# Kernel optimization log

Measured on AMD Instinct MI355X. Metric: run time of the kernel, lower is better.

The kernel has to match this reference:

```python
import jax, jax.numpy as jnp
import numpy as np

B, H, W, K, PAD = 1024, 28, 28, 3, 1


def conv3x3(x, w, b):
    out = jax.lax.conv_general_dilated(x, w, (1, 1), ((PAD, PAD), (PAD, PAD)),
                                       dimension_numbers=('NCHW', 'OIHW', 'NCHW'))
    return out + b[None, :, None, None]


def deform_conv2d(x, offset, w, b):
    # torchvision deform_conv2d semantics, stride=1, pad=1, dilation=1, groups=1
    Bn, Cin, Hh, Ww = x.shape
    Cout = w.shape[0]
    KK = K * K
    off = offset.reshape(Bn, KK, 2, Hh, Ww)
    dy, dx = off[:, :, 0], off[:, :, 1]                      # [B,KK,H,W]
    ky, kx = jnp.meshgrid(jnp.arange(K, dtype=x.dtype), jnp.arange(K, dtype=x.dtype), indexing='ij')
    py = dy + (jnp.arange(Hh, dtype=x.dtype) - PAD)[None, None, :, None] + ky.reshape(KK)[None, :, None, None]
    px = dx + (jnp.arange(Ww, dtype=x.dtype) - PAD)[None, None, None, :] + kx.reshape(KK)[None, :, None, None]
    y0 = jnp.floor(py); x0 = jnp.floor(px)
    wy1 = py - y0; wy0 = 1.0 - wy1
    wx1 = px - x0; wx0 = 1.0 - wx1
    xf = x.reshape(Bn, Cin, Hh * Ww)

    def gather(yi, xi):
        valid = (yi >= 0) & (yi < Hh) & (xi >= 0) & (xi < Ww)
        yc = jnp.clip(yi, 0, Hh - 1).astype(jnp.int32)
        xc = jnp.clip(xi, 0, Ww - 1).astype(jnp.int32)
        idx = (yc * Ww + xc).reshape(Bn, -1)                 # [B, KK*H*W]
        g = jnp.take_along_axis(xf, jnp.broadcast_to(idx[:, None, :], (Bn, Cin, idx.shape[1])), axis=2)
        return g.reshape(Bn, Cin, KK, Hh, Ww) * valid.astype(x.dtype)[:, None]

    sampled = (gather(y0, x0) * (wy0 * wx0)[:, None]
               + gather(y0, x0 + 1) * (wy0 * wx1)[:, None]
               + gather(y0 + 1, x0) * (wy1 * wx0)[:, None]
               + gather(y0 + 1, x0 + 1) * (wy1 * wx1)[:, None])  # [B,Cin,KK,H,W]
    out = jnp.einsum('bkhw,ok->bohw', sampled.reshape(Bn, Cin * KK, Hh, Ww),
                     w.reshape(Cout, Cin * KK))
    return out + b[None, :, None, None]


def adaptive_avg_pool_14(x):
    Bn, C, Hh, Ww = x.shape
    f = Hh // 14
    return x.reshape(Bn, C, 14, f, 14, f).mean(axis=(3, 5))


def setup_inputs() -> dict:
    key = jax.random.key(0)
    ks = jax.random.split(key, 14)
    d = {}
    d['x'] = jax.random.normal(ks[0], (B, 1, H, W), dtype=jnp.float32)
    # offset conv 1: Conv2d(1, 18, 3, pad=1)
    d['ow1'] = jax.random.normal(ks[1], (18, 1, 3, 3), dtype=jnp.float32) * 0.1
    d['ob1'] = jnp.zeros((18,), jnp.float32)
    d['w1'] = jax.random.normal(ks[2], (32, 1, 3, 3), dtype=jnp.float32) * 0.01
    d['b1'] = jnp.zeros((32,), jnp.float32)
    # offset conv 2: Conv2d(32, 18, 3, pad=1)
    d['ow2'] = jax.random.normal(ks[3], (18, 32, 3, 3), dtype=jnp.float32) * 0.05
    d['ob2'] = jnp.zeros((18,), jnp.float32)
    d['w2'] = jax.random.normal(ks[4], (64, 32, 3, 3), dtype=jnp.float32) * 0.01
    d['b2'] = jnp.zeros((64,), jnp.float32)
    d['fw1'] = jax.random.normal(ks[5], (128, 64 * 14 * 14), dtype=jnp.float32) * 0.01
    d['fb1'] = jnp.zeros((128,), jnp.float32)
    d['fw2'] = jax.random.normal(ks[6], (10, 128), dtype=jnp.float32) * 0.05
    d['fb2'] = jnp.zeros((10,), jnp.float32)
    return d


def reference(x, ow1, ob1, w1, b1, ow2, ob2, w2, b2, fw1, fb1, fw2, fb2):
    # block1 + relu + pool 28->14
    h = deform_conv2d(x, conv3x3(x, ow1, ob1), w1, b1)
    h = adaptive_avg_pool_14(jax.nn.relu(h))
    # block2 + relu + pool 14->14 (identity)
    h = deform_conv2d(h, conv3x3(h, ow2, ob2), w2, b2)
    h = adaptive_avg_pool_14(jax.nn.relu(h))
    h = h.reshape(h.shape[0], -1)
    # classifier (ExcitationDropout is identity in eval mode)
    h = jax.nn.relu(h @ fw1.T + fb1)
    return h @ fw2.T + fb2
```

## Files before the change

kernel.cpp:

```cpp
#include <hip/hip_runtime.h>

#define NB 1024
#define TOTAL1 (NB*196)
#define SP 208

#define WS_H1   0
#define WS_H2   6422528
#define WS_PART 19267584
#define WS_W1T  23461888
#define WS_OW1T 23462176
#define WS_W2T  23462338
#define WS_OW2T 23480770

__global__ __launch_bounds__(256) void prep(const float* __restrict__ w1,
                                            const float* __restrict__ ow1,
                                            const float* __restrict__ w2,
                                            const float* __restrict__ ow2,
                                            float* __restrict__ ws) {
  int i = blockIdx.x * 256 + threadIdx.x;
  if (i < 288)   { int co = i / 9,  kk = i % 9;   ws[WS_W1T  + kk * 32 + co] = w1[i]; }
  if (i < 162)   { int c  = i / 9,  j  = i % 9;   ws[WS_OW1T + j  * 18 + c ] = ow1[i]; }
  if (i < 18432) { int co = i / 288, k = i % 288; ws[WS_W2T  + k  * 64 + co] = w2[i]; }
  if (i < 5184)  { int c  = i / 288, k = i % 288; ws[WS_OW2T + k  * 18 + c ] = ow2[i]; }
}

__global__ __launch_bounds__(256, 2) void stage1(const float* __restrict__ x,
                                                 const float* __restrict__ ob1,
                                                 const float* __restrict__ b1,
                                                 const float* __restrict__ ws,
                                                 float* __restrict__ h1) {
  __shared__ float ximg[3 * 784];
  const float* __restrict__ w1t  = ws + WS_W1T;
  const float* __restrict__ ow1t = ws + WS_OW1T;
  int tid = threadIdx.x;
  int g0 = blockIdx.x * 256;
  int bfirst = g0 / 196;
  for (int idx = tid; idx < 3 * 784; idx += 256) {
    int img = idx / 784;
    int b = bfirst + img;
    ximg[idx] = (b < NB) ? x[b * 784 + (idx - img * 784)] : 0.f;
  }
  __syncthreads();
  int g = g0 + tid;
  if (g >= TOTAL1) return;
  int b = g / 196, p = g - b * 196;
  const float* im = ximg + (b - bfirst) * 784;
  int oy = p / 14, ox = p - (p / 14) * 14;

  float pooled[32];
#pragma unroll
  for (int co = 0; co < 32; ++co) pooled[co] = 0.f;

  for (int sub = 0; sub < 4; ++sub) {
    int y  = 2 * oy + (sub >> 1);
    int ix = 2 * ox + (sub & 1);
    float patch[9];
#pragma unroll
    for (int j = 0; j < 9; ++j) {
      int yy = y + j / 3 - 1, xc = ix + j % 3 - 1;
      bool ok = (yy >= 0) & (yy < 28) & (xc >= 0) & (xc < 28);
      patch[j] = ok ? im[yy * 28 + xc] : 0.f;
    }
    float off[18];
#pragma unroll
    for (int c = 0; c < 18; ++c) off[c] = ob1[c];
#pragma unroll
    for (int j = 0; j < 9; ++j) {
      float v = patch[j];
#pragma unroll
      for (int c = 0; c < 18; ++c) off[c] = fmaf(v, ow1t[j * 18 + c], off[c]);
    }
    float a[32];
#pragma unroll
    for (int co = 0; co < 32; ++co) a[co] = b1[co];
#pragma unroll
    for (int kk = 0; kk < 9; ++kk) {
      float py = (float)(y - 1 + kk / 3) + off[2 * kk];
      float px = (float)(ix - 1 + kk % 3) + off[2 * kk + 1];
      float y0f = floorf(py), x0f = floorf(px);
      float wy1 = py - y0f, wx1 = px - x0f;
      float wy0 = 1.f - wy1, wx0 = 1.f - wx1;
      int y0 = (int)y0f, x0 = (int)x0f;
      int y1 = y0 + 1, x1 = x0 + 1;
      bool vy0 = (y0 >= 0) & (y0 < 28), vy1 = (y1 >= 0) & (y1 < 28);
      bool vx0 = (x0 >= 0) & (x0 < 28), vx1 = (x1 >= 0) & (x1 < 28);
      float W00 = (vy0 & vx0) ? wy0 * wx0 : 0.f;
      float W01 = (vy0 & vx1) ? wy0 * wx1 : 0.f;
      float W10 = (vy1 & vx0) ? wy1 * wx0 : 0.f;
      float W11 = (vy1 & vx1) ? wy1 * wx1 : 0.f;
      int yc0 = min(max(y0, 0), 27), yc1 = min(max(y1, 0), 27);
      int xc0 = min(max(x0, 0), 27), xc1 = min(max(x1, 0), 27);
      float s = im[yc0 * 28 + xc0] * W00 + im[yc0 * 28 + xc1] * W01 +
                im[yc1 * 28 + xc0] * W10 + im[yc1 * 28 + xc1] * W11;
#pragma unroll
      for (int co = 0; co < 32; ++co) a[co] = fmaf(s, w1t[kk * 32 + co], a[co]);
    }
#pragma unroll
    for (int co = 0; co < 32; ++co) pooled[co] += fmaxf(a[co], 0.f);
  }
#pragma unroll
  for (int co = 0; co < 32; ++co) h1[b * 6272 + co * 196 + p] = pooled[co] * 0.25f;
}

__global__ __launch_bounds__(256, 2) void stage2(const float* __restrict__ h1,
                                                 const float* __restrict__ ob2,
                                                 const float* __restrict__ b2,
                                                 const float* __restrict__ ws,
                                                 float* __restrict__ h2) {
  __shared__ float imgT[196 * 32];
  __shared__ float offs[18 * SP];
  __shared__ float Sbuf[32 * SP];
  const float* __restrict__ w2t  = ws + WS_W2T;
  const float* __restrict__ ow2t = ws + WS_OW2T;
  int tid = threadIdx.x;
  int b = blockIdx.x;

  for (int e = tid; e < 6272; e += 256) {
    int ci = e / 196, p = e - ci * 196;
    imgT[p * 32 + ((ci + 4 * p) & 31)] = h1[b * 6272 + e];
  }

  int pp = tid;
  int spy = pp / 14, spx = pp - (pp / 14) * 14;

  int oc  = tid % 18;
  int opg = tid / 18;
  int op0 = opg * 16;
  bool oact = (tid < 234);
  float oacc[16];
#pragma unroll
  for (int i = 0; i < 16; ++i) oacc[i] = 0.f;

  for (int j = 0; j < 9; ++j) {
    __syncthreads();
    if (pp < SP) {
      if (pp < 196) {
        int yy = spy + j / 3 - 1, xx = spx + j % 3 - 1;
        bool ok = (yy >= 0) & (yy < 14) & (xx >= 0) & (xx < 14);
        int idx = ok ? (yy * 14 + xx) : 0;
        const float* src = imgT + idx * 32;
        int rot = (4 * idx) & 31;
#pragma unroll
        for (int cg = 0; cg < 8; ++cg) {
          float4 v;
          if (ok) v = *(const float4*)(src + ((cg * 4 + rot) & 31));
          else    v = make_float4(0.f, 0.f, 0.f, 0.f);
          Sbuf[(cg * 4 + 0) * SP + pp] = v.x;
          Sbuf[(cg * 4 + 1) * SP + pp] = v.y;
          Sbuf[(cg * 4 + 2) * SP + pp] = v.z;
          Sbuf[(cg * 4 + 3) * SP + pp] = v.w;
        }
      } else {
#pragma unroll
        for (int ci2 = 0; ci2 < 32; ++ci2) Sbuf[ci2 * SP + pp] = 0.f;
      }
    }
    __syncthreads();
    if (oact) {
      float wv[32];
#pragma unroll
      for (int ci2 = 0; ci2 < 32; ++ci2) wv[ci2] = ow2t[(ci2 * 9 + j) * 18 + oc];
      for (int ci2 = 0; ci2 < 32; ++ci2) {
        const float* srow = Sbuf + ci2 * SP + op0;
        float w = wv[ci2];
#pragma unroll
        for (int t = 0; t < 4; ++t) {
          float4 s = *(const float4*)(srow + 4 * t);
          oacc[4 * t + 0] = fmaf(w, s.x, oacc[4 * t + 0]);
          oacc[4 * t + 1] = fmaf(w, s.y, oacc[4 * t + 1]);
          oacc[4 * t + 2] = fmaf(w, s.z, oacc[4 * t + 2]);
          oacc[4 * t + 3] = fmaf(w, s.w, oacc[4 * t + 3]);
        }
      }
    }
  }
  __syncthreads();
  if (oact) {
    float bo = ob2[oc];
#pragma unroll
    for (int i = 0; i < 16; ++i) offs[oc * SP + op0 + i] = oacc[i] + bo;
  }

  int co = tid & 63, pg = tid >> 6;
  int p0 = pg * 52;
  float bb = b2[co];
  float acc[52];
#pragma unroll
  for (int i = 0; i < 52; ++i) acc[i] = bb;

  for (int kk = 0; kk < 9; ++kk) {
    __syncthreads();
    if (pp < SP) {
      if (pp < 196) {
        float dyv = offs[(2 * kk) * SP + pp];
        float dxv = offs[(2 * kk + 1) * SP + pp];
        float pyv = (float)(spy - 1 + kk / 3) + dyv;
        float pxv = (float)(spx - 1 + kk % 3) + dxv;
        float y0f = floorf(pyv), x0f = floorf(pxv);
        float wy1 = pyv - y0f, wx1 = pxv - x0f;
        float wy0 = 1.f - wy1, wx0 = 1.f - wx1;
        int y0 = (int)y0f, x0 = (int)x0f;
        int y1 = y0 + 1, x1 = x0 + 1;
        bool vy0 = (y0 >= 0) & (y0 < 14), vy1 = (y1 >= 0) & (y1 < 14);
        bool vx0 = (x0 >= 0) & (x0 < 14), vx1 = (x1 >= 0) & (x1 < 14);
        float W00 = (vy0 & vx0) ? wy0 * wx0 : 0.f;
        float W01 = (vy0 & vx1) ? wy0 * wx1 : 0.f;
        float W10 = (vy1 & vx0) ? wy1 * wx0 : 0.f;
        float W11 = (vy1 & vx1) ? wy1 * wx1 : 0.f;
        int yc0 = min(max(y0, 0), 13), yc1 = min(max(y1, 0), 13);
        int xc0 = min(max(x0, 0), 13), xc1 = min(max(x1, 0), 13);
        int i00 = yc0 * 14 + xc0, i01 = yc0 * 14 + xc1;
        int i10 = yc1 * 14 + xc0, i11 = yc1 * 14 + xc1;
        const float* s00 = imgT + i00 * 32; int r00 = (4 * i00) & 31;
        const float* s01 = imgT + i01 * 32; int r01 = (4 * i01) & 31;
        const float* s10 = imgT + i10 * 32; int r10 = (4 * i10) & 31;
        const float* s11 = imgT + i11 * 32; int r11 = (4 * i11) & 31;
#pragma unroll
        for (int cg = 0; cg < 8; ++cg) {
          float4 a0 = *(const float4*)(s00 + ((cg * 4 + r00) & 31));
          float4 a1 = *(const float4*)(s01 + ((cg * 4 + r01) & 31));
          float4 a2 = *(const float4*)(s10 + ((cg * 4 + r10) & 31));
          float4 a3 = *(const float4*)(s11 + ((cg * 4 + r11) & 31));
          float vx0v = fmaf(W00, a0.x, fmaf(W01, a1.x, fmaf(W10, a2.x, W11 * a3.x)));
          float vy0v = fmaf(W00, a0.y, fmaf(W01, a1.y, fmaf(W10, a2.y, W11 * a3.y)));
          float vz0v = fmaf(W00, a0.z, fmaf(W01, a1.z, fmaf(W10, a2.z, W11 * a3.z)));
          float vw0v = fmaf(W00, a0.w, fmaf(W01, a1.w, fmaf(W10, a2.w, W11 * a3.w)));
          Sbuf[(cg * 4 + 0) * SP + pp] = vx0v;
          Sbuf[(cg * 4 + 1) * SP + pp] = vy0v;
          Sbuf[(cg * 4 + 2) * SP + pp] = vz0v;
          Sbuf[(cg * 4 + 3) * SP + pp] = vw0v;
        }
      } else {
#pragma unroll
        for (int ci2 = 0; ci2 < 32; ++ci2) Sbuf[ci2 * SP + pp] = 0.f;
      }
    }
    __syncthreads();
    float wv[32];
#pragma unroll
    for (int ci2 = 0; ci2 < 32; ++ci2) wv[ci2] = w2t[(ci2 * 9 + kk) * 64 + co];
#pragma unroll 2
    for (int ci2 = 0; ci2 < 32; ++ci2) {
      const float* srow = Sbuf + ci2 * SP + p0;
      float w = wv[ci2];
#pragma unroll
      for (int t = 0; t < 13; ++t) {
        float4 s = *(const float4*)(srow + 4 * t);
        acc[4 * t + 0] = fmaf(w, s.x, acc[4 * t + 0]);
        acc[4 * t + 1] = fmaf(w, s.y, acc[4 * t + 1]);
        acc[4 * t + 2] = fmaf(w, s.z, acc[4 * t + 2]);
        acc[4 * t + 3] = fmaf(w, s.w, acc[4 * t + 3]);
      }
    }
  }

  for (int half = 0; half < 2; ++half) {
    __syncthreads();
    if ((co >> 5) == half) {
      int cc = co & 31;
#pragma unroll
      for (int i = 0; i < 52; ++i) Sbuf[cc * SP + p0 + i] = acc[i];
    }
    __syncthreads();
    for (int e = tid; e < 6272; e += 256) {
      int cc = e / 196, p = e - cc * 196;
      h2[b * 12544 + (half * 32 + cc) * 196 + p] = fmaxf(Sbuf[cc * SP + p], 0.f);
    }
  }
}

__global__ __launch_bounds__(256, 2) void fc1(const float* __restrict__ h2,
                                              const float* __restrict__ fw1,
                                              float* __restrict__ part) {
  __shared__ float a_s[56 * 72];
  __shared__ float b_s[56 * 132];
  int tid = threadIdx.x;
  int rb = (blockIdx.x & 15) * 64;
  int ks = blockIdx.x >> 4;
  int kbase = ks * 392;
  int c0 = (tid & 31) * 4;
  int r0 = (tid >> 5) * 8;

  float acc[8][4];
#pragma unroll
  for (int i = 0; i < 8; ++i)
#pragma unroll
    for (int j = 0; j < 4; ++j) acc[i][j] = 0.f;

  for (int ch = 0; ch < 7; ++ch) {
    int kb = kbase + ch * 56;
    __syncthreads();
#pragma unroll
    for (int t = 0; t < 14; ++t) {
      int idx = t * 256 + tid;
      int r = idx / 56, k = idx - r * 56;
      a_s[k * 72 + r] = h2[(rb + r) * 12544 + kb + k];
    }
#pragma unroll
    for (int t = 0; t < 28; ++t) {
      int idx = t * 256 + tid;
      int c = idx / 56, k = idx - c * 56;
      b_s[k * 132 + c] = fw1[c * 12544 + kb + k];
    }
    __syncthreads();
    for (int k = 0; k < 56; ++k) {
      float4 bv = *(const float4*)&b_s[k * 132 + c0];
      float4 av0 = *(const float4*)&a_s[k * 72 + r0];
      float4 av1 = *(const float4*)&a_s[k * 72 + r0 + 4];
      float av[8] = {av0.x, av0.y, av0.z, av0.w, av1.x, av1.y, av1.z, av1.w};
      float bj[4] = {bv.x, bv.y, bv.z, bv.w};
#pragma unroll
      for (int i = 0; i < 8; ++i)
#pragma unroll
        for (int j = 0; j < 4; ++j) acc[i][j] = fmaf(av[i], bj[j], acc[i][j]);
    }
  }
#pragma unroll
  for (int i = 0; i < 8; ++i) {
    int r = rb + r0 + i;
#pragma unroll
    for (int j = 0; j < 4; ++j)
      part[(ks * 1024 + r) * 128 + c0 + j] = acc[i][j];
  }
}

__global__ __launch_bounds__(128) void fcfinal(const float* __restrict__ part,
                                               const float* __restrict__ fb1,
                                               const float* __restrict__ fw2,
                                               const float* __restrict__ fb2,
                                               float* __restrict__ out) {
  __shared__ float tbuf[128];
  int b = blockIdx.x, c = threadIdx.x;
  float s = fb1[c];
  for (int ks = 0; ks < 32; ++ks) s += part[(ks * 1024 + b) * 128 + c];
  tbuf[c] = fmaxf(s, 0.f);
  __syncthreads();
  if (c < 10) {
    float v = fb2[c];
#pragma unroll
    for (int k = 0; k < 128; ++k) v = fmaf(tbuf[k], fw2[c * 128 + k], v);
    out[b * 10 + c] = v;
  }
}

extern "C" void kernel_launch(void* const* d_in, const int* in_sizes, int n_in,
                              void* d_out, int out_size, void* d_ws, size_t ws_size,
                              hipStream_t stream) {
  const float* x   = (const float*)d_in[0];
  const float* ow1 = (const float*)d_in[1];
  const float* ob1 = (const float*)d_in[2];
  const float* w1  = (const float*)d_in[3];
  const float* b1  = (const float*)d_in[4];
  const float* ow2 = (const float*)d_in[5];
  const float* ob2 = (const float*)d_in[6];
  const float* w2  = (const float*)d_in[7];
  const float* b2  = (const float*)d_in[8];
  const float* fw1 = (const float*)d_in[9];
  const float* fb1 = (const float*)d_in[10];
  const float* fw2 = (const float*)d_in[11];
  const float* fb2 = (const float*)d_in[12];
  float* ws  = (float*)d_ws;
  float* out = (float*)d_out;

  prep<<<72, 256, 0, stream>>>(w1, ow1, w2, ow2, ws);
  stage1<<<784, 256, 0, stream>>>(x, ob1, b1, ws, ws + WS_H1);
  stage2<<<NB, 256, 0, stream>>>(ws + WS_H1, ob2, b2, ws, ws + WS_H2);
  fc1<<<512, 256, 0, stream>>>(ws + WS_H2, fw1, ws + WS_PART);
  fcfinal<<<1024, 128, 0, stream>>>(ws + WS_PART, fb1, fw2, fb2, out);
}
```

Before: 424.5 us.

## Retile block2 deform-conv GEMM to 4x16 register tiles and store output directly

The block-2 channel-mix GEMM inside the deform conv kernel now gives each thread 4 output channels by 16 pixels instead of 1 channel by 52 pixels. Each shared-memory sample is reused across 4 weights, and the weights are loaded as float4 vectors. The aim is to cut LDS traffic per FMA. The final ReLU store now writes straight from registers to global memory with float4 stores, which removes the two-pass shared-memory staging and its barriers. In exchange, 48 of the 256 threads sit idle during the GEMM, and the global stores are less coalesced across channels.

```diff
diff --git a/kernel.cpp b/kernel.cpp
--- a/kernel.cpp
+++ b/kernel.cpp
@@ -181,12 +181,19 @@
     for (int i = 0; i < 16; ++i) offs[oc * SP + op0 + i] = oacc[i] + bo;
   }
 
-  int co = tid & 63, pg = tid >> 6;
-  int p0 = pg * 52;
-  float bb = b2[co];
-  float acc[52];
-#pragma unroll
-  for (int i = 0; i < 52; ++i) acc[i] = bb;
+  int cog = tid & 15, pg = tid >> 4;
+  int co0 = cog * 4;
+  int p0 = pg * 16;
+  bool gact = (pg < 13);
+  float acc[4][16];
+  {
+    float4 bb = *(const float4*)(b2 + co0);
+    float bj[4] = {bb.x, bb.y, bb.z, bb.w};
+#pragma unroll
+    for (int j = 0; j < 4; ++j)
+#pragma unroll
+      for (int i = 0; i < 16; ++i) acc[j][i] = bj[j];
+  }
 
   for (int kk = 0; kk < 9; ++kk) {
     __syncthreads();
@@ -221,14 +228,10 @@
           float4 a1 = *(const float4*)(s01 + ((cg * 4 + r01) & 31));
           float4 a2 = *(const float4*)(s10 + ((cg * 4 + r10) & 31));
           float4 a3 = *(const float4*)(s11 + ((cg * 4 + r11) & 31));
-          float vx0v = fmaf(W00, a0.x, fmaf(W01, a1.x, fmaf(W10, a2.x, W11 * a3.x)));
-          float vy0v = fmaf(W00, a0.y, fmaf(W01, a1.y, fmaf(W10, a2.y, W11 * a3.y)));
-          float vz0v = fmaf(W00, a0.z, fmaf(W01, a1.z, fmaf(W10, a2.z, W11 * a3.z)));
-          float vw0v = fmaf(W00, a0.w, fmaf(W01, a1.w, fmaf(W10, a2.w, W11 * a3.w)));
-          Sbuf[(cg * 4 + 0) * SP + pp] = vx0v;
-          Sbuf[(cg * 4 + 1) * SP + pp] = vy0v;
-          Sbuf[(cg * 4 + 2) * SP + pp] = vz0v;
-          Sbuf[(cg * 4 + 3) * SP + pp] = vw0v;
+          Sbuf[(cg * 4 + 0) * SP + pp] = fmaf(W00, a0.x, fmaf(W01, a1.x, fmaf(W10, a2.x, W11 * a3.x)));
+          Sbuf[(cg * 4 + 1) * SP + pp] = fmaf(W00, a0.y, fmaf(W01, a1.y, fmaf(W10, a2.y, W11 * a3.y)));
+          Sbuf[(cg * 4 + 2) * SP + pp] = fmaf(W00, a0.z, fmaf(W01, a1.z, fmaf(W10, a2.z, W11 * a3.z)));
+          Sbuf[(cg * 4 + 3) * SP + pp] = fmaf(W00, a0.w, fmaf(W01, a1.w, fmaf(W10, a2.w, W11 * a3.w)));
         }
       } else {
 #pragma unroll
@@ -236,35 +239,47 @@
       }
     }
     __syncthreads();
-    float wv[32];
-#pragma unroll
-    for (int ci2 = 0; ci2 < 32; ++ci2) wv[ci2] = w2t[(ci2 * 9 + kk) * 64 + co];
-#pragma unroll 2
-    for (int ci2 = 0; ci2 < 32; ++ci2) {
-      const float* srow = Sbuf + ci2 * SP + p0;
-      float w = wv[ci2];
-#pragma unroll
-      for (int t = 0; t < 13; ++t) {
-        float4 s = *(const float4*)(srow + 4 * t);
-        acc[4 * t + 0] = fmaf(w, s.x, acc[4 * t + 0]);
-        acc[4 * t + 1] = fmaf(w, s.y, acc[4 * t + 1]);
-        acc[4 * t + 2] = fmaf(w, s.z, acc[4 * t + 2]);
-        acc[4 * t + 3] = fmaf(w, s.w, acc[4 * t + 3]);
-      }
-    }
-  }
-
-  for (int half = 0; half < 2; ++half) {
-    __syncthreads();
-    if ((co >> 5) == half) {
-      int cc = co & 31;
-#pragma unroll
-      for (int i = 0; i < 52; ++i) Sbuf[cc * SP + p0 + i] = acc[i];
-    }
-    __syncthreads();
-    for (int e = tid; e < 6272; e += 256) {
-      int cc = e / 196, p = e - cc * 196;
-      h2[b * 12544 + (half * 32 + cc) * 196 + p] = fmaxf(Sbuf[cc * SP + p], 0.f);
+    if (gact) {
+      for (int cb = 0; cb < 32; cb += 8) {
+        float4 w[8];
+#pragma unroll
+        for (int u = 0; u < 8; ++u)
+          w[u] = *(const float4*)(w2t + ((cb + u) * 9 + kk) * 64 + co0);
+#pragma unroll
+        for (int u = 0; u < 8; ++u) {
+          const float* srow = Sbuf + (cb + u) * SP + p0;
+          float4 s0 = *(const float4*)(srow);
+          float4 s1 = *(const float4*)(srow + 4);
+          float4 s2 = *(const float4*)(srow + 8);
+          float4 s3 = *(const float4*)(srow + 12);
+          float sv[16] = {s0.x, s0.y, s0.z, s0.w, s1.x, s1.y, s1.z, s1.w,
+                          s2.x, s2.y, s2.z, s2.w, s3.x, s3.y, s3.z, s3.w};
+          float wj[4] = {w[u].x, w[u].y, w[u].z, w[u].w};
+#pragma unroll
+          for (int j = 0; j < 4; ++j)
+#pragma unroll
+            for (int i = 0; i < 16; ++i)
+              acc[j][i] = fmaf(wj[j], sv[i], acc[j][i]);
+        }
+      }
+    }
+  }
+
+  if (gact) {
+    float* __restrict__ orow = h2 + b * 12544 + co0 * 196 + p0;
+#pragma unroll
+    for (int j = 0; j < 4; ++j) {
+#pragma unroll
+      for (int t = 0; t < 4; ++t) {
+        if (p0 + 4 * t < 196) {
+          float4 v;
+          v.x = fmaxf(acc[j][4 * t + 0], 0.f);
+          v.y = fmaxf(acc[j][4 * t + 1], 0.f);
+          v.z = fmaxf(acc[j][4 * t + 2], 0.f);
+          v.w = fmaxf(acc[j][4 * t + 3], 0.f);
+          *(float4*)(orow + j * 196 + 4 * t) = v;
+        }
+      }
     }
   }
 }
```

Result: faster. 385.7 us (-9.1%).
